# Kernel tuning notes

Hardware: AMD Instinct MI355X
Metric: run time of the kernel (lower is better)

Reference implementation:

```python
import jax, jax.numpy as jnp
import numpy as np

def setup_inputs() -> dict:
    key = jax.random.key(0)
    ks = jax.random.split(key, 6)
    ch, cr = 256, 32  # cr = ch // 8
    B, H, W = 4, 64, 64
    sc = 1.0 / np.sqrt(ch)
    return {
        "inputs": jax.random.normal(ks[0], (B, H, W, ch), jnp.float32),
        "Wf": jax.random.normal(ks[1], (ch, cr), jnp.float32) * sc,
        "bf": jnp.zeros((cr,), jnp.float32),
        "Wg": jax.random.normal(ks[2], (ch, cr), jnp.float32) * sc,
        "bg": jnp.zeros((cr,), jnp.float32),
        "Wh": jax.random.normal(ks[3], (ch, cr), jnp.float32) * sc,
        "bh": jnp.zeros((cr,), jnp.float32),
        "Wv": jax.random.normal(ks[4], (cr, ch), jnp.float32) * (1.0 / np.sqrt(cr)),
        "bv": jnp.zeros((ch,), jnp.float32),
        "gamma": jnp.zeros((1,), jnp.float32),
    }

def reference(inputs, Wf, bf, Wg, bg, Wh, bh, Wv, bv, gamma):
    B, H, W, C = inputs.shape
    x = inputs.reshape(B, H * W, C)  # [B, N, C]
    f = x @ Wf + bf  # [B, N, cr] (keys)
    g = x @ Wg + bg  # [B, N, cr] (queries)
    h = x @ Wh + bh  # [B, N, cr] (values)
    s = jnp.einsum('bnk,bmk->bnm', g, f)  # [B, N, N]
    beta = jax.nn.softmax(s, axis=-1)
    v = jnp.einsum('bnm,bmk->bnk', beta, h)  # [B, N, cr]
    o = v @ Wv + bv  # [B, N, C]
    out = gamma * o + x
    return out.reshape(B, H, W, C)
```

## Files before the change

kernel.cpp:

```cpp
#include <hip/hip_runtime.h>

#define B_SZ  4
#define N_TOK 4096
#define CH    256
#define CR    32
#define SEG   512
#define KT    64
#define NITER (SEG / KT)
#define LOG2E 1.44269504f

typedef __attribute__((ext_vector_type(8))) short bf16x8;
typedef __attribute__((ext_vector_type(4))) float f32x4;

__device__ inline ushort f2bf(float x) {
    uint u = __float_as_uint(x);
    u += 0x7fff + ((u >> 16) & 1);
    return (ushort)(u >> 16);
}
__device__ inline uint pk2bf(float a, float b) {
    return __builtin_amdgcn_perm(__float_as_uint(b), __float_as_uint(a), 0x07060302);
}
__device__ inline float fast_exp2(float x) {
#if __has_builtin(__builtin_amdgcn_exp2f)
    return __builtin_amdgcn_exp2f(x);
#else
    return exp2f(x);
#endif
}

__global__ __launch_bounds__(256) void prep_kernel(
    const float* __restrict__ Wf, const float* __restrict__ Wg,
    const float* __restrict__ Wh, const float* __restrict__ Wv,
    ushort* __restrict__ wft, ushort* __restrict__ wgt,
    ushort* __restrict__ wht, ushort* __restrict__ wvt)
{
    int t = threadIdx.x, blk = blockIdx.x;
    if (blk < 3) {
        const float* W  = (blk == 0) ? Wf : (blk == 1) ? Wg : Wh;
        ushort*      Wt = (blk == 0) ? wft : (blk == 1) ? wgt : wht;
        int j = t & 31, half = t >> 5;
        ushort tmp[32];
        #pragma unroll
        for (int kk = 0; kk < 32; ++kk)
            tmp[kk] = f2bf(W[(half * 32 + kk) * CR + j]);
        ushort* dst = Wt + (size_t)j * CH + half * 32;
        #pragma unroll
        for (int k8 = 0; k8 < 4; ++k8)
            *(bf16x8*)(dst + k8 * 8) = *(bf16x8*)&tmp[k8 * 8];
    } else {
        ushort tmp[32];
        #pragma unroll
        for (int k = 0; k < CR; ++k) tmp[k] = f2bf(Wv[k * CH + t]);
        ushort* dst = wvt + (size_t)t * CR;
        #pragma unroll
        for (int k8 = 0; k8 < 4; ++k8)
            *(bf16x8*)(dst + k8 * 8) = *(bf16x8*)&tmp[k8 * 8];
    }
}

__global__ __launch_bounds__(256) void proj_kernel(
    const float* __restrict__ x,
    const ushort* __restrict__ wft, const ushort* __restrict__ wgt, const ushort* __restrict__ wht,
    const float* __restrict__ bf_, const float* __restrict__ bg, const float* __restrict__ bh,
    ushort* __restrict__ fo, ushort* __restrict__ go, ushort* __restrict__ hto)
{
    __shared__ f32x4 accx[3][6][64];
    int t  = threadIdx.x;
    int wv = t >> 6, L = t & 63, nl = L & 15, Q = L >> 4;
    int row_t = blockIdx.x * 16;
    int b = row_t >> 12, tok0 = row_t & 4095;

    const float* xrow = x + (size_t)(row_t + nl) * CH;
    f32x4 A[6];
    #pragma unroll
    for (int i = 0; i < 6; ++i) A[i] = (f32x4){0.f, 0.f, 0.f, 0.f};

    #pragma unroll
    for (int c2 = 0; c2 < 2; ++c2) {
        int off = wv * 64 + c2 * 32 + Q * 8;
        float4 lo = *(const float4*)(xrow + off);
        float4 hi = *(const float4*)(xrow + off + 4);
        bf16x8 xa;
        xa[0] = (short)f2bf(lo.x); xa[1] = (short)f2bf(lo.y);
        xa[2] = (short)f2bf(lo.z); xa[3] = (short)f2bf(lo.w);
        xa[4] = (short)f2bf(hi.x); xa[5] = (short)f2bf(hi.y);
        xa[6] = (short)f2bf(hi.z); xa[7] = (short)f2bf(hi.w);

        bf16x8 wf0 = *(const bf16x8*)(wft + (size_t)nl * CH + off);
        bf16x8 wf1 = *(const bf16x8*)(wft + (size_t)(16 + nl) * CH + off);
        bf16x8 wg0 = *(const bf16x8*)(wgt + (size_t)nl * CH + off);
        bf16x8 wg1 = *(const bf16x8*)(wgt + (size_t)(16 + nl) * CH + off);
        bf16x8 wh0 = *(const bf16x8*)(wht + (size_t)nl * CH + off);
        bf16x8 wh1 = *(const bf16x8*)(wht + (size_t)(16 + nl) * CH + off);

        A[0] = __builtin_amdgcn_mfma_f32_16x16x32_bf16(xa, wf0, A[0], 0, 0, 0);
        A[1] = __builtin_amdgcn_mfma_f32_16x16x32_bf16(xa, wf1, A[1], 0, 0, 0);
        A[2] = __builtin_amdgcn_mfma_f32_16x16x32_bf16(xa, wg0, A[2], 0, 0, 0);
        A[3] = __builtin_amdgcn_mfma_f32_16x16x32_bf16(xa, wg1, A[3], 0, 0, 0);
        A[4] = __builtin_amdgcn_mfma_f32_16x16x32_bf16(wh0, xa, A[4], 0, 0, 0);
        A[5] = __builtin_amdgcn_mfma_f32_16x16x32_bf16(wh1, xa, A[5], 0, 0, 0);
    }

    if (wv > 0) {
        #pragma unroll
        for (int i = 0; i < 6; ++i) accx[wv - 1][i][L] = A[i];
    }
    __syncthreads();
    if (wv == 0) {
        #pragma unroll
        for (int i = 0; i < 6; ++i) {
            f32x4 s0 = accx[0][i][L], s1 = accx[1][i][L], s2 = accx[2][i][L];
            A[i] = A[i] + s0 + s1 + s2;
        }
        float bF0 = bf_[nl], bF1 = bf_[16 + nl];
        float bG0 = bg[nl] * LOG2E, bG1 = bg[16 + nl] * LOG2E;
        #pragma unroll
        for (int r = 0; r < 4; ++r) {
            size_t ro = (size_t)(row_t + Q * 4 + r) * CR;
            fo[ro + nl]      = f2bf(A[0][r] + bF0);
            fo[ro + 16 + nl] = f2bf(A[1][r] + bF1);
            go[ro + nl]      = f2bf(fmaf(A[2][r], LOG2E, bG0));
            go[ro + 16 + nl] = f2bf(fmaf(A[3][r], LOG2E, bG1));
        }
        ushort* hb = hto + (size_t)b * CR * N_TOK + tok0 + nl;
        #pragma unroll
        for (int r = 0; r < 4; ++r) {
            int ch = Q * 4 + r;
            hb[(size_t)ch * N_TOK]        = f2bf(A[4][r] + bh[ch]);
            hb[(size_t)(16 + ch) * N_TOK] = f2bf(A[5][r] + bh[16 + ch]);
        }
    }
}

__global__ __launch_bounds__(512, 4) void attn_kernel(
    const ushort* __restrict__ f, const ushort* __restrict__ g,
    const ushort* __restrict__ ht, const ushort* __restrict__ wvt,
    const float* __restrict__ bv, const float* __restrict__ gamma,
    const float* __restrict__ x, float* __restrict__ out)
{
    __shared__ unsigned long long smem_raw[38912 / 8];
    ushort (*pls)[32][76]  = (ushort (*)[32][76])smem_raw;
    float  (*obuf)[32][33] = (float (*)[32][33])smem_raw;
    float  (*lbuf)[32]     = (float (*)[32])((char*)smem_raw + 33792);
    ushort (*oc)[48]       = (ushort (*)[48])((char*)smem_raw + 34816);

    int t  = threadIdx.x;
    int wv = t >> 6;
    int L  = t & 63;
    int nl = L & 15;
    int Q  = L >> 4;
    int bid = blockIdx.x;
    int swz = (bid & 7) * 64 + (bid >> 3);
    int b  = swz >> 7;
    int q0 = (swz & 127) * 32;

    const ushort* fb  = f  + (size_t)b * N_TOK * CR;
    const ushort* htb = ht + (size_t)b * CR * N_TOK;

    bf16x8 gB0 = *(const bf16x8*)(g + ((size_t)b * N_TOK + q0 + nl) * CR + Q * 8);
    bf16x8 gB1 = *(const bf16x8*)(g + ((size_t)b * N_TOK + q0 + 16 + nl) * CR + Q * 8);

    f32x4 acc00 = {0,0,0,0}, acc01 = {0,0,0,0};
    f32x4 acc10 = {0,0,0,0}, acc11 = {0,0,0,0};
    const f32x4 zf = {0,0,0,0};
    float lsum0 = 0.f, lsum1 = 0.f;

    int key0 = wv * SEG;
    bf16x8 Ac0 = *(const bf16x8*)(fb + (size_t)(key0 +  0 + nl) * CR + Q * 8);
    bf16x8 Ac1 = *(const bf16x8*)(fb + (size_t)(key0 + 16 + nl) * CR + Q * 8);
    bf16x8 Ac2 = *(const bf16x8*)(fb + (size_t)(key0 + 32 + nl) * CR + Q * 8);
    bf16x8 Ac3 = *(const bf16x8*)(fb + (size_t)(key0 + 48 + nl) * CR + Q * 8);

    #pragma unroll 2
    for (int it = 0; it < NITER; ++it) {
        int kc = wv * SEG + it * KT;
        const ushort* hk = htb + (size_t)nl * N_TOK + kc;
        bf16x8 b00 = *(const bf16x8*)(hk + Q * 8);
        bf16x8 b01 = *(const bf16x8*)(hk + (size_t)16 * N_TOK + Q * 8);
        bf16x8 b10 = *(const bf16x8*)(hk + 32 + Q * 8);
        bf16x8 b11 = *(const bf16x8*)(hk + (size_t)16 * N_TOK + 32 + Q * 8);
        int kn = wv * SEG + ((it + 1 < NITER) ? it + 1 : 0) * KT;
        const ushort* fn = fb + (size_t)kn * CR;
        bf16x8 An0 = *(const bf16x8*)(fn + (size_t)( 0 + nl) * CR + Q * 8);
        bf16x8 An1 = *(const bf16x8*)(fn + (size_t)(16 + nl) * CR + Q * 8);
        bf16x8 An2 = *(const bf16x8*)(fn + (size_t)(32 + nl) * CR + Q * 8);
        bf16x8 An3 = *(const bf16x8*)(fn + (size_t)(48 + nl) * CR + Q * 8);

        f32x4 s00 = __builtin_amdgcn_mfma_f32_16x16x32_bf16(Ac0, gB0, zf, 0, 0, 0);
        f32x4 s01 = __builtin_amdgcn_mfma_f32_16x16x32_bf16(Ac1, gB0, zf, 0, 0, 0);
        f32x4 s02 = __builtin_amdgcn_mfma_f32_16x16x32_bf16(Ac2, gB0, zf, 0, 0, 0);
        f32x4 s03 = __builtin_amdgcn_mfma_f32_16x16x32_bf16(Ac3, gB0, zf, 0, 0, 0);
        f32x4 s10 = __builtin_amdgcn_mfma_f32_16x16x32_bf16(Ac0, gB1, zf, 0, 0, 0);
        f32x4 s11 = __builtin_amdgcn_mfma_f32_16x16x32_bf16(Ac1, gB1, zf, 0, 0, 0);
        f32x4 s12 = __builtin_amdgcn_mfma_f32_16x16x32_bf16(Ac2, gB1, zf, 0, 0, 0);
        f32x4 s13 = __builtin_amdgcn_mfma_f32_16x16x32_bf16(Ac3, gB1, zf, 0, 0, 0);

        #pragma unroll
        for (int qh = 0; qh < 2; ++qh) {
            f32x4 v0 = qh ? s10 : s00, v1 = qh ? s11 : s01;
            f32x4 v2 = qh ? s12 : s02, v3 = qh ? s13 : s03;
            int row = qh * 16 + nl;
            float p0 = fast_exp2(v0[0]), p1 = fast_exp2(v0[1]);
            float p2 = fast_exp2(v0[2]), p3 = fast_exp2(v0[3]);
            float s4 = ((p0+p1)+(p2+p3));
            uint2 w; w.x = pk2bf(p0,p1); w.y = pk2bf(p2,p3);
            *(uint2*)&pls[wv][row][ 0 + Q * 4] = w;
            p0 = fast_exp2(v1[0]); p1 = fast_exp2(v1[1]);
            p2 = fast_exp2(v1[2]); p3 = fast_exp2(v1[3]);
            s4 += ((p0+p1)+(p2+p3));
            w.x = pk2bf(p0,p1); w.y = pk2bf(p2,p3);
            *(uint2*)&pls[wv][row][16 + Q * 4] = w;
            p0 = fast_exp2(v2[0]); p1 = fast_exp2(v2[1]);
            p2 = fast_exp2(v2[2]); p3 = fast_exp2(v2[3]);
            s4 += ((p0+p1)+(p2+p3));
            w.x = pk2bf(p0,p1); w.y = pk2bf(p2,p3);
            *(uint2*)&pls[wv][row][32 + Q * 4] = w;
            p0 = fast_exp2(v3[0]); p1 = fast_exp2(v3[1]);
            p2 = fast_exp2(v3[2]); p3 = fast_exp2(v3[3]);
            s4 += ((p0+p1)+(p2+p3));
            w.x = pk2bf(p0,p1); w.y = pk2bf(p2,p3);
            *(uint2*)&pls[wv][row][48 + Q * 4] = w;
            if (qh) lsum1 += s4; else lsum0 += s4;
        }

        bf16x8 aP00 = *(const bf16x8*)&pls[wv][     nl][ 0 + Q * 8];
        bf16x8 aP01 = *(const bf16x8*)&pls[wv][     nl][32 + Q * 8];
        bf16x8 aP10 = *(const bf16x8*)&pls[wv][16 + nl][ 0 + Q * 8];
        bf16x8 aP11 = *(const bf16x8*)&pls[wv][16 + nl][32 + Q * 8];

        acc00 = __builtin_amdgcn_mfma_f32_16x16x32_bf16(aP00, b00, acc00, 0, 0, 0);
        acc01 = __builtin_amdgcn_mfma_f32_16x16x32_bf16(aP00, b01, acc01, 0, 0, 0);
        acc10 = __builtin_amdgcn_mfma_f32_16x16x32_bf16(aP10, b00, acc10, 0, 0, 0);
        acc11 = __builtin_amdgcn_mfma_f32_16x16x32_bf16(aP10, b01, acc11, 0, 0, 0);
        acc00 = __builtin_amdgcn_mfma_f32_16x16x32_bf16(aP01, b10, acc00, 0, 0, 0);
        acc01 = __builtin_amdgcn_mfma_f32_16x16x32_bf16(aP01, b11, acc01, 0, 0, 0);
        acc10 = __builtin_amdgcn_mfma_f32_16x16x32_bf16(aP11, b10, acc10, 0, 0, 0);
        acc11 = __builtin_amdgcn_mfma_f32_16x16x32_bf16(aP11, b11, acc11, 0, 0, 0);

        Ac0 = An0; Ac1 = An1; Ac2 = An2; Ac3 = An3;
    }

    lsum0 += __shfl_xor(lsum0, 16); lsum0 += __shfl_xor(lsum0, 32);
    lsum1 += __shfl_xor(lsum1, 16); lsum1 += __shfl_xor(lsum1, 32);

    __syncthreads();
    #pragma unroll
    for (int r = 0; r < 4; ++r) {
        obuf[wv][     Q * 4 + r][nl]      = acc00[r];
        obuf[wv][     Q * 4 + r][16 + nl] = acc01[r];
        obuf[wv][16 + Q * 4 + r][nl]      = acc10[r];
        obuf[wv][16 + Q * 4 + r][16 + nl] = acc11[r];
    }
    if (L < 16) { lbuf[wv][nl] = lsum0; lbuf[wv][16 + nl] = lsum1; }
    __syncthreads();

    {
        int ch = t & 31, qb = t >> 5;
        #pragma unroll
        for (int qq = qb; qq < 32; qq += 16) {
            float s = 0.f, Lq = 0.f;
            #pragma unroll
            for (int w = 0; w < 8; ++w) { s += obuf[w][qq][ch]; Lq += lbuf[w][qq]; }
            oc[qq][ch] = f2bf(s / Lq);
        }
    }
    __syncthreads();

    bf16x8 aO0 = *(const bf16x8*)&oc[     nl][Q * 8];
    bf16x8 aO1 = *(const bf16x8*)&oc[16 + nl][Q * 8];
    float gm = gamma[0];
    const float* xb = x   + ((size_t)b * N_TOK + q0) * CH;
    float*       ob = out + ((size_t)b * N_TOK + q0) * CH;
    #pragma unroll
    for (int i = 0; i < 2; ++i) {
        int nb = wv * 2 + i;
        bf16x8 bW = *(const bf16x8*)(wvt + (size_t)(nb * 16 + nl) * CR + Q * 8);
        f32x4 d0 = __builtin_amdgcn_mfma_f32_16x16x32_bf16(aO0, bW, zf, 0, 0, 0);
        f32x4 d1 = __builtin_amdgcn_mfma_f32_16x16x32_bf16(aO1, bW, zf, 0, 0, 0);
        int c = nb * 16 + nl;
        float bvc = bv[c];
        #pragma unroll
        for (int r = 0; r < 4; ++r) {
            int qa = Q * 4 + r;
            ob[qa * CH + c]        = fmaf(gm, d0[r] + bvc, xb[qa * CH + c]);
            ob[(16 + qa) * CH + c] = fmaf(gm, d1[r] + bvc, xb[(16 + qa) * CH + c]);
        }
    }
}

extern "C" void kernel_launch(void* const* d_in, const int* in_sizes, int n_in,
                              void* d_out, int out_size, void* d_ws, size_t ws_size,
                              hipStream_t stream) {
    const float* x     = (const float*)d_in[0];
    const float* Wf    = (const float*)d_in[1];
    const float* bf_   = (const float*)d_in[2];
    const float* Wg    = (const float*)d_in[3];
    const float* bg    = (const float*)d_in[4];
    const float* Wh    = (const float*)d_in[5];
    const float* bh    = (const float*)d_in[6];
    const float* Wv    = (const float*)d_in[7];
    const float* bv    = (const float*)d_in[8];
    const float* gamma = (const float*)d_in[9];
    float* out = (float*)d_out;

    const size_t T = (size_t)B_SZ * N_TOK * CR;
    ushort* fo  = (ushort*)d_ws;
    ushort* go  = fo + T;
    ushort* hto = go + T;
    ushort* wvt = hto + T;
    ushort* wft = wvt + CH * CR;
    ushort* wgt = wft + CH * CR;
    ushort* wht = wgt + CH * CR;

    prep_kernel<<<4, 256, 0, stream>>>(Wf, Wg, Wh, Wv, wft, wgt, wht, wvt);
    proj_kernel<<<B_SZ * N_TOK / 16, 256, 0, stream>>>(x, wft, wgt, wht, bf_, bg, bh, fo, go, hto);
    attn_kernel<<<B_SZ * (N_TOK / 32), 512, 0, stream>>>(fo, go, hto, wvt, bv, gamma, x, out);
}
```

Before: 125.6 us.

## Fold weight prep into projection and attention kernels, drop prep launch

```diff
diff --git a/kernel.cpp b/kernel.cpp
--- a/kernel.cpp
+++ b/kernel.cpp
@@ -28,46 +28,35 @@
 #endif
 }
 
-__global__ __launch_bounds__(256) void prep_kernel(
-    const float* __restrict__ Wf, const float* __restrict__ Wg,
-    const float* __restrict__ Wh, const float* __restrict__ Wv,
-    ushort* __restrict__ wft, ushort* __restrict__ wgt,
-    ushort* __restrict__ wht, ushort* __restrict__ wvt)
-{
-    int t = threadIdx.x, blk = blockIdx.x;
-    if (blk < 3) {
-        const float* W  = (blk == 0) ? Wf : (blk == 1) ? Wg : Wh;
-        ushort*      Wt = (blk == 0) ? wft : (blk == 1) ? wgt : wht;
-        int j = t & 31, half = t >> 5;
-        ushort tmp[32];
-        #pragma unroll
-        for (int kk = 0; kk < 32; ++kk)
-            tmp[kk] = f2bf(W[(half * 32 + kk) * CR + j]);
-        ushort* dst = Wt + (size_t)j * CH + half * 32;
-        #pragma unroll
-        for (int k8 = 0; k8 < 4; ++k8)
-            *(bf16x8*)(dst + k8 * 8) = *(bf16x8*)&tmp[k8 * 8];
-    } else {
-        ushort tmp[32];
-        #pragma unroll
-        for (int k = 0; k < CR; ++k) tmp[k] = f2bf(Wv[k * CH + t]);
-        ushort* dst = wvt + (size_t)t * CR;
-        #pragma unroll
-        for (int k8 = 0; k8 < 4; ++k8)
-            *(bf16x8*)(dst + k8 * 8) = *(bf16x8*)&tmp[k8 * 8];
-    }
-}
-
 __global__ __launch_bounds__(256) void proj_kernel(
     const float* __restrict__ x,
-    const ushort* __restrict__ wft, const ushort* __restrict__ wgt, const ushort* __restrict__ wht,
+    const float* __restrict__ Wf, const float* __restrict__ Wg, const float* __restrict__ Wh,
     const float* __restrict__ bf_, const float* __restrict__ bg, const float* __restrict__ bh,
     ushort* __restrict__ fo, ushort* __restrict__ go, ushort* __restrict__ hto)
 {
-    __shared__ f32x4 accx[3][6][64];
-    int t  = threadIdx.x;
+    __shared__ ushort wst[3][32][264];
+    int t = threadIdx.x;
+
+    {
+        float4 r4[8];
+        const float* rf = (const float*)&r4[0];
+        #pragma unroll
+        for (int q4 = 0; q4 < 8; ++q4) r4[q4] = *(const float4*)(Wf + (size_t)t * CR + q4 * 4);
+        #pragma unroll
+        for (int j = 0; j < 32; ++j) wst[0][j][t] = f2bf(rf[j]);
+        #pragma unroll
+        for (int q4 = 0; q4 < 8; ++q4) r4[q4] = *(const float4*)(Wg + (size_t)t * CR + q4 * 4);
+        #pragma unroll
+        for (int j = 0; j < 32; ++j) wst[1][j][t] = f2bf(rf[j]);
+        #pragma unroll
+        for (int q4 = 0; q4 < 8; ++q4) r4[q4] = *(const float4*)(Wh + (size_t)t * CR + q4 * 4);
+        #pragma unroll
+        for (int j = 0; j < 32; ++j) wst[2][j][t] = f2bf(rf[j]);
+    }
+    __syncthreads();
+
     int wv = t >> 6, L = t & 63, nl = L & 15, Q = L >> 4;
-    int row_t = blockIdx.x * 16;
+    int row_t = blockIdx.x * 64 + wv * 16;
     int b = row_t >> 12, tok0 = row_t & 4095;
 
     const float* xrow = x + (size_t)(row_t + nl) * CH;
@@ -76,8 +65,8 @@
     for (int i = 0; i < 6; ++i) A[i] = (f32x4){0.f, 0.f, 0.f, 0.f};
 
     #pragma unroll
-    for (int c2 = 0; c2 < 2; ++c2) {
-        int off = wv * 64 + c2 * 32 + Q * 8;
+    for (int kk = 0; kk < 8; ++kk) {
+        int off = kk * 32 + Q * 8;
         float4 lo = *(const float4*)(xrow + off);
         float4 hi = *(const float4*)(xrow + off + 4);
         bf16x8 xa;
@@ -86,12 +75,12 @@
         xa[4] = (short)f2bf(hi.x); xa[5] = (short)f2bf(hi.y);
         xa[6] = (short)f2bf(hi.z); xa[7] = (short)f2bf(hi.w);
 
-        bf16x8 wf0 = *(const bf16x8*)(wft + (size_t)nl * CH + off);
-        bf16x8 wf1 = *(const bf16x8*)(wft + (size_t)(16 + nl) * CH + off);
-        bf16x8 wg0 = *(const bf16x8*)(wgt + (size_t)nl * CH + off);
-        bf16x8 wg1 = *(const bf16x8*)(wgt + (size_t)(16 + nl) * CH + off);
-        bf16x8 wh0 = *(const bf16x8*)(wht + (size_t)nl * CH + off);
-        bf16x8 wh1 = *(const bf16x8*)(wht + (size_t)(16 + nl) * CH + off);
+        bf16x8 wf0 = *(const bf16x8*)&wst[0][nl][off];
+        bf16x8 wf1 = *(const bf16x8*)&wst[0][16 + nl][off];
+        bf16x8 wg0 = *(const bf16x8*)&wst[1][nl][off];
+        bf16x8 wg1 = *(const bf16x8*)&wst[1][16 + nl][off];
+        bf16x8 wh0 = *(const bf16x8*)&wst[2][nl][off];
+        bf16x8 wh1 = *(const bf16x8*)&wst[2][16 + nl][off];
 
         A[0] = __builtin_amdgcn_mfma_f32_16x16x32_bf16(xa, wf0, A[0], 0, 0, 0);
         A[1] = __builtin_amdgcn_mfma_f32_16x16x32_bf16(xa, wf1, A[1], 0, 0, 0);
@@ -101,40 +90,28 @@
         A[5] = __builtin_amdgcn_mfma_f32_16x16x32_bf16(wh1, xa, A[5], 0, 0, 0);
     }
 
-    if (wv > 0) {
-        #pragma unroll
-        for (int i = 0; i < 6; ++i) accx[wv - 1][i][L] = A[i];
-    }
-    __syncthreads();
-    if (wv == 0) {
-        #pragma unroll
-        for (int i = 0; i < 6; ++i) {
-            f32x4 s0 = accx[0][i][L], s1 = accx[1][i][L], s2 = accx[2][i][L];
-            A[i] = A[i] + s0 + s1 + s2;
-        }
-        float bF0 = bf_[nl], bF1 = bf_[16 + nl];
-        float bG0 = bg[nl] * LOG2E, bG1 = bg[16 + nl] * LOG2E;
-        #pragma unroll
-        for (int r = 0; r < 4; ++r) {
-            size_t ro = (size_t)(row_t + Q * 4 + r) * CR;
-            fo[ro + nl]      = f2bf(A[0][r] + bF0);
-            fo[ro + 16 + nl] = f2bf(A[1][r] + bF1);
-            go[ro + nl]      = f2bf(fmaf(A[2][r], LOG2E, bG0));
-            go[ro + 16 + nl] = f2bf(fmaf(A[3][r], LOG2E, bG1));
-        }
-        ushort* hb = hto + (size_t)b * CR * N_TOK + tok0 + nl;
-        #pragma unroll
-        for (int r = 0; r < 4; ++r) {
-            int ch = Q * 4 + r;
-            hb[(size_t)ch * N_TOK]        = f2bf(A[4][r] + bh[ch]);
-            hb[(size_t)(16 + ch) * N_TOK] = f2bf(A[5][r] + bh[16 + ch]);
-        }
+    float bF0 = bf_[nl], bF1 = bf_[16 + nl];
+    float bG0 = bg[nl] * LOG2E, bG1 = bg[16 + nl] * LOG2E;
+    #pragma unroll
+    for (int r = 0; r < 4; ++r) {
+        size_t ro = (size_t)(row_t + Q * 4 + r) * CR;
+        fo[ro + nl]      = f2bf(A[0][r] + bF0);
+        fo[ro + 16 + nl] = f2bf(A[1][r] + bF1);
+        go[ro + nl]      = f2bf(fmaf(A[2][r], LOG2E, bG0));
+        go[ro + 16 + nl] = f2bf(fmaf(A[3][r], LOG2E, bG1));
+    }
+    ushort* hb = hto + (size_t)b * CR * N_TOK + tok0 + nl;
+    #pragma unroll
+    for (int r = 0; r < 4; ++r) {
+        int ch = Q * 4 + r;
+        hb[(size_t)ch * N_TOK]        = f2bf(A[4][r] + bh[ch]);
+        hb[(size_t)(16 + ch) * N_TOK] = f2bf(A[5][r] + bh[16 + ch]);
     }
 }
 
 __global__ __launch_bounds__(512, 4) void attn_kernel(
     const ushort* __restrict__ f, const ushort* __restrict__ g,
-    const ushort* __restrict__ ht, const ushort* __restrict__ wvt,
+    const ushort* __restrict__ ht, const float* __restrict__ Wv,
     const float* __restrict__ bv, const float* __restrict__ gamma,
     const float* __restrict__ x, float* __restrict__ out)
 {
@@ -274,10 +251,13 @@
     #pragma unroll
     for (int i = 0; i < 2; ++i) {
         int nb = wv * 2 + i;
-        bf16x8 bW = *(const bf16x8*)(wvt + (size_t)(nb * 16 + nl) * CR + Q * 8);
+        int c = nb * 16 + nl;
+        const float* wvp = Wv + c;
+        bf16x8 bW;
+        #pragma unroll
+        for (int j = 0; j < 8; ++j) bW[j] = (short)f2bf(wvp[(size_t)(Q * 8 + j) * CH]);
         f32x4 d0 = __builtin_amdgcn_mfma_f32_16x16x32_bf16(aO0, bW, zf, 0, 0, 0);
         f32x4 d1 = __builtin_amdgcn_mfma_f32_16x16x32_bf16(aO1, bW, zf, 0, 0, 0);
-        int c = nb * 16 + nl;
         float bvc = bv[c];
         #pragma unroll
         for (int r = 0; r < 4; ++r) {
@@ -307,12 +287,7 @@
     ushort* fo  = (ushort*)d_ws;
     ushort* go  = fo + T;
     ushort* hto = go + T;
-    ushort* wvt = hto + T;
-    ushort* wft = wvt + CH * CR;
-    ushort* wgt = wft + CH * CR;
-    ushort* wht = wgt + CH * CR;
-
-    prep_kernel<<<4, 256, 0, stream>>>(Wf, Wg, Wh, Wv, wft, wgt, wht, wvt);
-    proj_kernel<<<B_SZ * N_TOK / 16, 256, 0, stream>>>(x, wft, wgt, wht, bf_, bg, bh, fo, go, hto);
-    attn_kernel<<<B_SZ * (N_TOK / 32), 512, 0, stream>>>(fo, go, hto, wvt, bv, gamma, x, out);
-}
+
+    proj_kernel<<<B_SZ * N_TOK / 64, 256, 0, stream>>>(x, Wf, Wg, Wh, bf_, bg, bh, fo, go, hto);
+    attn_kernel<<<B_SZ * (N_TOK / 32), 512, 0, stream>>>(fo, go, hto, Wv, bv, gamma, x, out);
+}
```

New measurement: 120.8 us. 1.04x faster.
